# Performance work log

Measured on AMD Instinct MI355X. Metric: run time of the kernel, lower is better.

The kernel has to match this reference:

```python
import jax, jax.numpy as jnp
import numpy as np

INPUT_DIM, QK_DIM, V_DIM = 1024, 512, 512

def setup_inputs() -> dict:
    key = jax.random.key(0)
    ks = jax.random.split(key, 7)
    B, S = 4, 2048
    scale = 1.0 / np.sqrt(INPUT_DIM)
    return {
        "x": jax.random.normal(ks[0], (B, S, INPUT_DIM), dtype=jnp.float32),
        "Wq": jax.random.normal(ks[1], (INPUT_DIM, QK_DIM), dtype=jnp.float32) * scale,
        "bq": jax.random.normal(ks[2], (QK_DIM,), dtype=jnp.float32) * 0.01,
        "Wk": jax.random.normal(ks[3], (INPUT_DIM, QK_DIM), dtype=jnp.float32) * scale,
        "bk": jax.random.normal(ks[4], (QK_DIM,), dtype=jnp.float32) * 0.01,
        "Wv": jax.random.normal(ks[5], (INPUT_DIM, V_DIM), dtype=jnp.float32) * scale,
        "bv": jax.random.normal(ks[6], (V_DIM,), dtype=jnp.float32) * 0.01,
    }

def reference(x, Wq, bq, Wk, bk, Wv, bv):
    # q,k: (B,S,Dqk), v: (B,S,Dv)
    q = jnp.einsum("bsi,id->bsd", x, Wq) + bq
    k = jnp.einsum("bsi,id->bsd", x, Wk) + bk
    v = jnp.einsum("bsi,id->bsd", x, Wv) + bv
    scale = 1.0 / jnp.sqrt(jnp.asarray(q.shape[-1], q.dtype))
    scores = jnp.einsum("bqd,bkd->bqk", q, k) * scale  # (B,S,S)
    attn = jax.nn.softmax(scores, axis=-1)
    return jnp.einsum("bqk,bkd->bqd", attn, v)
```

## Files before the change

kernel.cpp:

```cpp
#include <hip/hip_runtime.h>

typedef __attribute__((ext_vector_type(8))) short short8;
typedef __attribute__((ext_vector_type(4))) float f32x4;

#define S_    2048
#define DI    1024
#define DQK   512
#define DV    512
#define NTOK  8192

#define GLL(gp, lp) __builtin_amdgcn_global_load_lds( \
    (const __attribute__((address_space(1))) unsigned int*)(gp), \
    (__attribute__((address_space(3))) unsigned int*)(lp), 16, 0, 0)

static __device__ __forceinline__ unsigned short f2bf(float f) {
  unsigned int u = __float_as_uint(f);
  u += 0x7fffu + ((u >> 16) & 1u);
  return (unsigned short)(u >> 16);
}

__global__ void conv_all_kernel(const float* __restrict__ x,
                                const float* __restrict__ W0, const float* __restrict__ W1,
                                const float* __restrict__ W2,
                                unsigned short* __restrict__ xb,
                                unsigned short* __restrict__ T0, unsigned short* __restrict__ T1,
                                unsigned short* __restrict__ T2,
                                float* __restrict__ rowsum) {
  int z = blockIdx.z;
  if (z >= 3) {
    int blk = (z - 3) * 512 + blockIdx.y * 16 + blockIdx.x;
    int idx = (blk * 256 + threadIdx.x) * 8;
    const float4* p = (const float4*)(x + idx);
    float4 f0 = p[0], f1 = p[1];
    uint4 o;
    o.x = (unsigned)f2bf(f0.x) | ((unsigned)f2bf(f0.y) << 16);
    o.y = (unsigned)f2bf(f0.z) | ((unsigned)f2bf(f0.w) << 16);
    o.z = (unsigned)f2bf(f1.x) | ((unsigned)f2bf(f1.y) << 16);
    o.w = (unsigned)f2bf(f1.z) | ((unsigned)f2bf(f1.w) << 16);
    *(uint4*)(xb + idx) = o;
    return;
  }
  __shared__ float tile[32][33];
  int mat = z;
  if (mat == 0 && blockIdx.x == 0)
    rowsum[blockIdx.y * 256 + threadIdx.x] = 0.f;
  const float* W = (mat == 0) ? W0 : (mat == 1) ? W1 : W2;
  unsigned short* T = (mat == 0) ? T0 : (mat == 1) ? T1 : T2;
  int n0 = blockIdx.x * 32, k0 = blockIdx.y * 32;
  int c = threadIdx.x & 31, r0 = threadIdx.x >> 5;
  for (int i = 0; i < 4; ++i) {
    int kk = r0 + i * 8;
    tile[kk][c] = W[(k0 + kk) * DQK + n0 + c];
  }
  __syncthreads();
  for (int i = 0; i < 4; ++i) {
    int nn = r0 + i * 8;
    T[(n0 + nn) * DI + k0 + c] = f2bf(tile[c][nn]);
  }
}

template<int NSTAGE>
__device__ __forceinline__ void gemm_core_128x128(
    const unsigned short* __restrict__ A, const unsigned short* __restrict__ B,
    int lda, int ldb, int K, int m0, int n0,
    unsigned short* As, unsigned short* Bs, f32x4 (&acc)[4][4]) {
  int tid = threadIdx.x, lane = tid & 63, wv = tid >> 6;
  int quad = lane >> 4, l16 = lane & 15;
  int wm = wv >> 1, wn = wv & 1;
  int r0 = wv * 32 + (lane >> 2);
  int c8 = ((lane & 3) ^ ((lane >> 2) & 3)) * 8;
  const unsigned short* ga0 = A + (size_t)(m0 + r0) * lda + c8;
  const unsigned short* ga1 = ga0 + (size_t)16 * lda;
  const unsigned short* gb0 = B + (size_t)(n0 + r0) * ldb + c8;
  const unsigned short* gb1 = gb0 + (size_t)16 * ldb;
  int ldsw0 = (wv * 32) * 32;
  int ldsw1 = ldsw0 + 16 * 32;
#pragma unroll
  for (int i = 0; i < 4; ++i)
#pragma unroll
    for (int j = 0; j < 4; ++j) acc[i][j] = (f32x4){0.f, 0.f, 0.f, 0.f};

  auto stage = [&](int buf, int k0) {
    unsigned short* Ad = As + buf * (128 * 32);
    unsigned short* Bd = Bs + buf * (128 * 32);
    GLL(ga0 + k0, Ad + ldsw0);
    GLL(ga1 + k0, Ad + ldsw1);
    GLL(gb0 + k0, Bd + ldsw0);
    GLL(gb1 + k0, Bd + ldsw1);
  };

  int nk = K >> 5;
  int pc = (quad ^ (l16 & 3)) * 8;
#pragma unroll
  for (int s = 0; s < NSTAGE; ++s) stage(s, s * 32);
  int cur = 0, pre = NSTAGE;
  for (int kt = 0; kt < nk; ++kt) {
    if (kt + NSTAGE <= nk) {
      if constexpr (NSTAGE == 2) { asm volatile("s_waitcnt vmcnt(4)" ::: "memory"); }
      else                       { asm volatile("s_waitcnt vmcnt(12)" ::: "memory"); }
    } else {
      asm volatile("s_waitcnt vmcnt(0)" ::: "memory");
    }
    __builtin_amdgcn_sched_barrier(0);
    __builtin_amdgcn_s_barrier();
    __builtin_amdgcn_sched_barrier(0);
    if (kt + NSTAGE < nk) stage(pre, (kt + NSTAGE) * 32);
    __builtin_amdgcn_sched_barrier(0);
    const unsigned short* Ab = As + cur * (128 * 32);
    const unsigned short* Bb = Bs + cur * (128 * 32);
    short8 af[4], bf[4];
#pragma unroll
    for (int t = 0; t < 4; ++t) {
      af[t] = *(const short8*)(Ab + (wm * 64 + t * 16 + l16) * 32 + pc);
      bf[t] = *(const short8*)(Bb + (wn * 64 + t * 16 + l16) * 32 + pc);
    }
#pragma unroll
    for (int tm = 0; tm < 4; ++tm)
#pragma unroll
      for (int tn = 0; tn < 4; ++tn)
        acc[tm][tn] = __builtin_amdgcn_mfma_f32_16x16x32_bf16(af[tm], bf[tn], acc[tm][tn], 0, 0, 0);
    cur = (cur == NSTAGE) ? 0 : cur + 1;
    pre = (pre == NSTAGE) ? 0 : pre + 1;
  }
}

__global__ __launch_bounds__(256, 2) void qkv_dma_kernel(
    const unsigned short* __restrict__ xb,
    const unsigned short* __restrict__ wqt, const unsigned short* __restrict__ wkt,
    const unsigned short* __restrict__ wvt,
    const float* __restrict__ bq, const float* __restrict__ bk, const float* __restrict__ bv,
    unsigned short* __restrict__ qo, unsigned short* __restrict__ ko,
    unsigned short* __restrict__ vto) {
  __shared__ unsigned short As[3 * 128 * 32];
  __shared__ unsigned short Bs[3 * 128 * 32];
  int bidx = blockIdx.x;
  int xcd = bidx & 7;
  int local = bidx >> 3;
  int mlocal = local & 7;
  int col12 = local >> 3;
  int mat = col12 >> 2;
  int m0 = (xcd * 8 + mlocal) * 128;
  int n0 = (col12 & 3) * 128;
  const unsigned short* wt = (mat == 0) ? wqt : (mat == 1) ? wkt : wvt;
  const float* bias = (mat == 0) ? bq : (mat == 1) ? bk : bv;
  float oscale = (mat == 0) ? 0.04419417382415922f : 1.0f;
  f32x4 acc[4][4];
  gemm_core_128x128<2>(xb, wt, DI, DI, DI, m0, n0, As, Bs, acc);

  int tid = threadIdx.x, lane = tid & 63, wv = tid >> 6;
  int quad = lane >> 4, l16 = lane & 15;
  int wm = wv >> 1, wn = wv & 1;
  bool transp = (mat == 2);
  unsigned short* outp = (mat == 0) ? qo : (mat == 1) ? ko : vto;
#pragma unroll
  for (int tn = 0; tn < 4; ++tn) {
    int col = n0 + wn * 64 + tn * 16 + l16;
    float bc = bias[col];
#pragma unroll
    for (int tm = 0; tm < 4; ++tm) {
      int rowb = m0 + wm * 64 + tm * 16 + quad * 4;
      f32x4 a = acc[tm][tn];
      if (!transp) {
        outp[(size_t)(rowb + 0) * DQK + col] = f2bf((a.x + bc) * oscale);
        outp[(size_t)(rowb + 1) * DQK + col] = f2bf((a.y + bc) * oscale);
        outp[(size_t)(rowb + 2) * DQK + col] = f2bf((a.z + bc) * oscale);
        outp[(size_t)(rowb + 3) * DQK + col] = f2bf((a.w + bc) * oscale);
      } else {
        ushort4 pk;
        pk.x = f2bf(a.x + bc); pk.y = f2bf(a.y + bc);
        pk.z = f2bf(a.z + bc); pk.w = f2bf(a.w + bc);
        *(ushort4*)(outp + (size_t)col * NTOK + rowb) = pk;
      }
    }
  }
}

__global__ __launch_bounds__(512, 1) void s_exp_kernel(
    const unsigned short* __restrict__ q, const unsigned short* __restrict__ k,
    unsigned short* __restrict__ sp, float* __restrict__ rowsum) {
  __shared__ unsigned short As[2 * 256 * 32];
  __shared__ unsigned short Bs[2 * 256 * 32];
  int bidx = blockIdx.x;
  int xcd = bidx & 7, b = xcd >> 1, p = xcd & 1;
  int local = bidx >> 3;
  int m0 = (p * 4 + (local & 3)) * 256;
  int n0 = (local >> 2) * 256;
  const unsigned short* A = k + (size_t)b * S_ * DQK;
  const unsigned short* B = q + (size_t)b * S_ * DQK;

  int tid = threadIdx.x, lane = tid & 63, wv = tid >> 6;
  int quad = lane >> 4, l16 = lane & 15;
  int wm = wv >> 2, wn = wv & 3;
  int r0 = wv * 32 + (lane >> 2);
  int c8 = ((lane & 3) ^ ((lane >> 2) & 3)) * 8;
  const unsigned short* ga0 = A + (size_t)(m0 + r0) * DQK + c8;
  const unsigned short* ga1 = ga0 + (size_t)16 * DQK;
  const unsigned short* gb0 = B + (size_t)(n0 + r0) * DQK + c8;
  const unsigned short* gb1 = gb0 + (size_t)16 * DQK;
  int ldsw0 = (wv * 32) * 32;
  int ldsw1 = ldsw0 + 16 * 32;

  f32x4 acc[8][4];
#pragma unroll
  for (int i = 0; i < 8; ++i)
#pragma unroll
    for (int j = 0; j < 4; ++j) acc[i][j] = (f32x4){0.f, 0.f, 0.f, 0.f};

  auto stage = [&](int buf, int k0) {
    GLL(ga0 + k0, As + buf * 8192 + ldsw0);
    GLL(ga1 + k0, As + buf * 8192 + ldsw1);
    GLL(gb0 + k0, Bs + buf * 8192 + ldsw0);
    GLL(gb1 + k0, Bs + buf * 8192 + ldsw1);
  };

  int pc = (quad ^ (l16 & 3)) * 8;
  stage(0, 0);
  for (int kt = 0; kt < 16; ++kt) {
    int cur = kt & 1;
    __syncthreads();
    if (kt + 1 < 16) stage(cur ^ 1, (kt + 1) * 32);
    const unsigned short* Ab = As + cur * 8192;
    const unsigned short* Bb = Bs + cur * 8192;
    short8 af[8], bf[4];
#pragma unroll
    for (int t = 0; t < 8; ++t)
      af[t] = *(const short8*)(Ab + (wm * 128 + t * 16 + l16) * 32 + pc);
#pragma unroll
    for (int t = 0; t < 4; ++t)
      bf[t] = *(const short8*)(Bb + (wn * 64 + t * 16 + l16) * 32 + pc);
#pragma unroll
    for (int tm = 0; tm < 8; ++tm)
#pragma unroll
      for (int tn = 0; tn < 4; ++tn)
        acc[tm][tn] = __builtin_amdgcn_mfma_f32_16x16x32_bf16(af[tm], bf[tn], acc[tm][tn], 0, 0, 0);
  }

  unsigned short* Cb = sp + (size_t)b * S_ * S_;
#pragma unroll
  for (int tn = 0; tn < 4; ++tn) {
    int qrow = n0 + wn * 64 + tn * 16 + l16;
    float rs = 0.f;
#pragma unroll
    for (int tm = 0; tm < 8; ++tm) {
      int kcol = m0 + wm * 128 + tm * 16 + quad * 4;
      f32x4 a = acc[tm][tn];
      float e0 = __expf(a.x), e1 = __expf(a.y), e2 = __expf(a.z), e3 = __expf(a.w);
      ushort4 pk;
      pk.x = f2bf(e0); pk.y = f2bf(e1); pk.z = f2bf(e2); pk.w = f2bf(e3);
      *(ushort4*)(Cb + (size_t)qrow * S_ + kcol) = pk;
      rs += (e0 + e1) + (e2 + e3);
    }
    rs += __shfl_xor(rs, 16);
    rs += __shfl_xor(rs, 32);
    if (quad == 0) atomicAdd(rowsum + b * S_ + qrow, rs);
  }
}

__global__ __launch_bounds__(256, 2) void pv_kernel(
    const unsigned short* __restrict__ sp, const unsigned short* __restrict__ vt,
    const float* __restrict__ rowsum, float* __restrict__ out) {
  __shared__ unsigned short As[3 * 128 * 32];
  __shared__ unsigned short Bs[3 * 128 * 32];
  int bidx = blockIdx.x;
  int xcd = bidx & 7, b = xcd >> 1;
  int local = bidx >> 3;
  int m0 = (((xcd & 1) << 3) | (local >> 2)) * 128;
  int n0 = (local & 3) * 128;
  f32x4 acc[4][4];
  gemm_core_128x128<2>(sp + (size_t)b * S_ * S_, vt + (size_t)b * S_,
                       S_, NTOK, S_, m0, n0, As, Bs, acc);

  int tid = threadIdx.x, lane = tid & 63, wv = tid >> 6;
  int quad = lane >> 4, l16 = lane & 15;
  int wm = wv >> 1, wn = wv & 1;
  float* ob = out + (size_t)b * S_ * DV;
#pragma unroll
  for (int tm = 0; tm < 4; ++tm) {
    int rowb = m0 + wm * 64 + tm * 16 + quad * 4;
    float inv[4];
#pragma unroll
    for (int i = 0; i < 4; ++i) inv[i] = 1.0f / rowsum[b * S_ + rowb + i];
#pragma unroll
    for (int tn = 0; tn < 4; ++tn) {
      int col = n0 + wn * 64 + tn * 16 + l16;
      f32x4 a = acc[tm][tn];
      ob[(size_t)(rowb + 0) * DV + col] = a.x * inv[0];
      ob[(size_t)(rowb + 1) * DV + col] = a.y * inv[1];
      ob[(size_t)(rowb + 2) * DV + col] = a.z * inv[2];
      ob[(size_t)(rowb + 3) * DV + col] = a.w * inv[3];
    }
  }
}

extern "C" void kernel_launch(void* const* d_in, const int* in_sizes, int n_in,
                              void* d_out, int out_size, void* d_ws, size_t ws_size,
                              hipStream_t stream) {
  const float* x  = (const float*)d_in[0];
  const float* Wq = (const float*)d_in[1];
  const float* bq = (const float*)d_in[2];
  const float* Wk = (const float*)d_in[3];
  const float* bk = (const float*)d_in[4];
  const float* Wv = (const float*)d_in[5];
  const float* bv = (const float*)d_in[6];
  float* out = (float*)d_out;

  char* ws = (char*)d_ws;
  unsigned short* xb  = (unsigned short*)(ws);
  unsigned short* wqt = (unsigned short*)(ws + 16777216);
  unsigned short* wkt = (unsigned short*)(ws + 16777216 + 1048576);
  unsigned short* wvt = (unsigned short*)(ws + 16777216 + 2097152);
  unsigned short* qo  = (unsigned short*)(ws + 19922944);
  unsigned short* ko  = (unsigned short*)(ws + 19922944 + 8388608);
  unsigned short* vto = (unsigned short*)(ws + 19922944 + 16777216);
  unsigned short* sp  = (unsigned short*)(ws + 45088768);
  float* rowsum       = (float*)(ws + 45088768 + 33554432);

  dim3 gc(16, 32, 11);
  conv_all_kernel<<<gc, 256, 0, stream>>>(x, Wq, Wk, Wv, xb, wqt, wkt, wvt, rowsum);
  qkv_dma_kernel<<<768, 256, 0, stream>>>(xb, wqt, wkt, wvt, bq, bk, bv, qo, ko, vto);
  s_exp_kernel<<<256, 512, 0, stream>>>(qo, ko, sp, rowsum);
  pv_kernel<<<256, 256, 0, stream>>>(sp, vto, rowsum, out);
}
```

Measured before the change: 192.5 us.

## Shrink PV GEMM tiles to 64x64 with custom double-buffered loop

Replaces the shared 128x128 GEMM core in the P·V kernel with an inline 64x64 tile loop that uses two LDS buffers, a 64-wide K step and XOR-swizzled async global-to-LDS loads. The grid grows from 256 to 1024 blocks, with launch bounds raised to allow 4 blocks per CU. The aim is better CU utilisation on MI355X, where 256 blocks underfill the device. In exchange each tile reuses less data, so more bytes of P and V^T are loaded from global memory, and the loop has only two stages of buffering.

```diff
diff --git a/kernel.cpp b/kernel.cpp
--- a/kernel.cpp
+++ b/kernel.cpp
@@ -256,33 +256,75 @@
   }
 }
 
-__global__ __launch_bounds__(256, 2) void pv_kernel(
+__global__ __launch_bounds__(256, 4) void pv_kernel(
     const unsigned short* __restrict__ sp, const unsigned short* __restrict__ vt,
     const float* __restrict__ rowsum, float* __restrict__ out) {
-  __shared__ unsigned short As[3 * 128 * 32];
-  __shared__ unsigned short Bs[3 * 128 * 32];
+  __shared__ unsigned short As[2][64 * 64];
+  __shared__ unsigned short Bs[2][64 * 64];
   int bidx = blockIdx.x;
   int xcd = bidx & 7, b = xcd >> 1;
-  int local = bidx >> 3;
-  int m0 = (((xcd & 1) << 3) | (local >> 2)) * 128;
-  int n0 = (local & 3) * 128;
-  f32x4 acc[4][4];
-  gemm_core_128x128<2>(sp + (size_t)b * S_ * S_, vt + (size_t)b * S_,
-                       S_, NTOK, S_, m0, n0, As, Bs, acc);
-
+  int sub = ((bidx >> 3) << 1) | (xcd & 1);
+  int m0 = (sub >> 3) * 64, n0 = (sub & 7) * 64;
   int tid = threadIdx.x, lane = tid & 63, wv = tid >> 6;
   int quad = lane >> 4, l16 = lane & 15;
   int wm = wv >> 1, wn = wv & 1;
+  const unsigned short* A = sp + (size_t)b * S_ * S_;
+  const unsigned short* B = vt + (size_t)b * S_;
+
+  int srow = tid >> 3;
+  int schunk = (tid & 7) ^ (srow & 7);
+  const unsigned short* gA0 = A + (size_t)(m0 + srow) * S_ + schunk * 8;
+  const unsigned short* gA1 = A + (size_t)(m0 + 32 + srow) * S_ + schunk * 8;
+  const unsigned short* gB0 = B + (size_t)(n0 + srow) * NTOK + schunk * 8;
+  const unsigned short* gB1 = B + (size_t)(n0 + 32 + srow) * NTOK + schunk * 8;
+  int ldsw0 = (wv * 8) * 64;
+  int ldsw1 = (32 + wv * 8) * 64;
+
+  f32x4 acc[2][2];
+#pragma unroll
+  for (int i = 0; i < 2; ++i)
+#pragma unroll
+    for (int j = 0; j < 2; ++j) acc[i][j] = (f32x4){0.f, 0.f, 0.f, 0.f};
+
+  auto stage = [&](int buf, int k0) {
+    GLL(gA0 + k0, &As[buf][ldsw0]);
+    GLL(gA1 + k0, &As[buf][ldsw1]);
+    GLL(gB0 + k0, &Bs[buf][ldsw0]);
+    GLL(gB1 + k0, &Bs[buf][ldsw1]);
+  };
+
+  stage(0, 0);
+  for (int kt = 0; kt < 32; ++kt) {
+    int cur = kt & 1;
+    __syncthreads();
+    if (kt + 1 < 32) stage(cur ^ 1, (kt + 1) * 64);
+#pragma unroll
+    for (int ks = 0; ks < 2; ++ks) {
+      int pc = ((ks * 4 + quad) ^ (l16 & 7)) * 8;
+      short8 af[2], bf[2];
+#pragma unroll
+      for (int t = 0; t < 2; ++t) {
+        af[t] = *(const short8*)(&As[cur][(wm * 32 + t * 16 + l16) * 64 + pc]);
+        bf[t] = *(const short8*)(&Bs[cur][(wn * 32 + t * 16 + l16) * 64 + pc]);
+      }
+#pragma unroll
+      for (int tm = 0; tm < 2; ++tm)
+#pragma unroll
+        for (int tn = 0; tn < 2; ++tn)
+          acc[tm][tn] = __builtin_amdgcn_mfma_f32_16x16x32_bf16(af[tm], bf[tn], acc[tm][tn], 0, 0, 0);
+    }
+  }
+
   float* ob = out + (size_t)b * S_ * DV;
 #pragma unroll
-  for (int tm = 0; tm < 4; ++tm) {
-    int rowb = m0 + wm * 64 + tm * 16 + quad * 4;
+  for (int tm = 0; tm < 2; ++tm) {
+    int rowb = m0 + wm * 32 + tm * 16 + quad * 4;
     float inv[4];
 #pragma unroll
     for (int i = 0; i < 4; ++i) inv[i] = 1.0f / rowsum[b * S_ + rowb + i];
 #pragma unroll
-    for (int tn = 0; tn < 4; ++tn) {
-      int col = n0 + wn * 64 + tn * 16 + l16;
+    for (int tn = 0; tn < 2; ++tn) {
+      int col = n0 + wn * 32 + tn * 16 + l16;
       f32x4 a = acc[tm][tn];
       ob[(size_t)(rowb + 0) * DV + col] = a.x * inv[0];
       ob[(size_t)(rowb + 1) * DV + col] = a.y * inv[1];
@@ -319,5 +361,5 @@
   conv_all_kernel<<<gc, 256, 0, stream>>>(x, Wq, Wk, Wv, xb, wqt, wkt, wvt, rowsum);
   qkv_dma_kernel<<<768, 256, 0, stream>>>(xb, wqt, wkt, wvt, bq, bk, bv, qo, ko, vto);
   s_exp_kernel<<<256, 512, 0, stream>>>(qo, ko, sp, rowsum);
-  pv_kernel<<<256, 256, 0, stream>>>(sp, vto, rowsum, out);
-}
+  pv_kernel<<<1024, 256, 0, stream>>>(sp, vto, rowsum, out);
+}
```

Result: faster. 180.9 us (-6.1%).
